# Performance work log

Measured on AMD Instinct MI355X. Metric: run time of the kernel, lower is better.

Reference implementation:

```python
import jax, jax.numpy as jnp
import numpy as np
from jax import lax

LAM = 1.0
B, L = 64, 512
WORD_DIM, POS_DIM, HIDDEN = 256, 32, 768
D_E = 3 * WORD_DIM            # 768, Xe feature dim
D_P = 2 * POS_DIM + WORD_DIM  # 320, Xp feature dim

# fixed piecewise-pool mask table: row 0 = padding, rows 1..3 = segments
MASK_TABLE = jnp.array([[0, 0, 0], [1, 0, 0], [0, 1, 0], [0, 0, 1]], dtype=jnp.float32)


def setup_inputs() -> dict:
    key = jax.random.key(0)
    ks = jax.random.split(key, 9)
    s1 = 1.0 / np.sqrt(D_E)
    s2 = 1.0 / np.sqrt(D_P)
    sc = 1.0 / np.sqrt(D_E * 3)
    return {
        "Xp": jax.random.normal(ks[0], (B, L, D_P), jnp.float32),
        "Xe": jax.random.normal(ks[1], (B, L, D_E), jnp.float32),
        "X_mask": jax.random.randint(ks[2], (B, L), 0, 4, jnp.int32),
        "W1": jax.random.uniform(ks[3], (D_E, D_E), jnp.float32, -s1, s1),
        "b1": jax.random.uniform(ks[4], (D_E,), jnp.float32, -s1, s1),
        "W2": jax.random.uniform(ks[5], (D_E, D_P), jnp.float32, -s2, s2),
        "b2": jax.random.uniform(ks[6], (D_E,), jnp.float32, -s2, s2),
        "Wc": jax.random.uniform(ks[7], (HIDDEN, D_E, 3), jnp.float32, -sc, sc),
        "bc": jax.random.uniform(ks[8], (HIDDEN,), jnp.float32, -sc, sc),
    }


def _forward(Xp, Xe, W1, b1, W2, b2, Wc, bc, X_mask):
    # gated linear fusion of entity and position features
    A = jax.nn.sigmoid(jnp.einsum('bld,od->blo', Xe / LAM, W1) + b1)   # [B,L,D_E]
    X = A * Xe + (1.0 - A) * jnp.tanh(jnp.einsum('bld,od->blo', Xp, W2) + b2)
    # conv1d over length, padding=1 (same)
    x_ncl = jnp.transpose(X, (0, 2, 1))                                 # [B,D_E,L]
    y = lax.conv_general_dilated(x_ncl, Wc, window_strides=(1,),
                                 padding=((1, 1),),
                                 dimension_numbers=('NCH', 'OIH', 'NCH'))
    y = jnp.transpose(y + bc[None, :, None], (0, 2, 1))                 # [B,L,H]
    # piecewise max pooling: mask-multiply then max over L, per segment
    m = MASK_TABLE[X_mask]                                              # [B,L,3]
    pooled = jnp.stack([jnp.max(y * m[:, :, k:k + 1], axis=1) for k in range(3)],
                       axis=-1)                                         # [B,H,3]
    return jnp.tanh(pooled.reshape(-1, HIDDEN * 3))                     # [B,3H]


def reference(Xp, Xe, X_mask, W1, b1, W2, b2, Wc, bc):
    return _forward(Xp, Xe, W1, b1, W2, b2, Wc, bc, X_mask)
```

## Files before the change

kernel.cpp:

```cpp
#include <hip/hip_runtime.h>
#include <math.h>

#define DE 768
#define DP 320
#define HID 768
#define LL 512
#define BB 64
#define M_TOT (BB * LL)
#define HD (HID * DE)

typedef _Float16 half8 __attribute__((ext_vector_type(8)));
typedef _Float16 half4 __attribute__((ext_vector_type(4)));
typedef _Float16 half2v __attribute__((ext_vector_type(2)));
typedef float floatx4 __attribute__((ext_vector_type(4)));

__device__ __forceinline__ void gload16(const void* g, void* l) {
    __builtin_amdgcn_global_load_lds(
        (const __attribute__((address_space(1))) unsigned int*)g,
        (__attribute__((address_space(3))) unsigned int*)l, 16, 0, 0);
}

__device__ __forceinline__ float fast_sigmoid(float x) {
    return __builtin_amdgcn_rcpf(1.f + __expf(-x));
}
__device__ __forceinline__ float fast_tanh(float x) {
    return 2.f * __builtin_amdgcn_rcpf(1.f + __expf(-2.f * x)) - 1.f;
}

__device__ __forceinline__ unsigned fkey(float v) {
    unsigned u = __float_as_uint(v);
    return (u & 0x80000000u) ? ~u : (u | 0x80000000u);
}
__device__ __forceinline__ float funkey(unsigned k) {
    unsigned u = (k & 0x80000000u) ? (k & 0x7FFFFFFFu) : ~k;
    return __uint_as_float(u);
}

__global__ __launch_bounds__(256) void prep_all(
    const float* __restrict__ Xe, const float* __restrict__ W1,
    const float* __restrict__ W2, const float* __restrict__ Wc,
    _Float16* __restrict__ Xe_h, _Float16* __restrict__ W1_h,
    _Float16* __restrict__ W2_h, _Float16* __restrict__ WcT)
{
    const int bid = blockIdx.x, tid = threadIdx.x;
    if (bid < 24576) {
        int idx = bid * 256 + tid;
        float4 v = ((const float4*)Xe)[idx];
        half4 h = {(_Float16)v.x, (_Float16)v.y, (_Float16)v.z, (_Float16)v.w};
        *(half4*)&Xe_h[(size_t)idx * 4] = h;
    } else if (bid < 25152) {
        int idx = (bid - 24576) * 256 + tid;
        float4 v = ((const float4*)W1)[idx];
        half4 h = {(_Float16)v.x, (_Float16)v.y, (_Float16)v.z, (_Float16)v.w};
        *(half4*)&W1_h[(size_t)idx * 4] = h;
    } else if (bid < 25392) {
        int idx = (bid - 25152) * 256 + tid;
        float4 v = ((const float4*)W2)[idx];
        half4 h = {(_Float16)v.x, (_Float16)v.y, (_Float16)v.z, (_Float16)v.w};
        *(half4*)&W2_h[(size_t)idx * 4] = h;
    } else {
        int idx = (bid - 25392) * 256 + tid;
        float a = Wc[(size_t)idx * 3 + 0];
        float b = Wc[(size_t)idx * 3 + 1];
        float c = Wc[(size_t)idx * 3 + 2];
        WcT[idx]          = (_Float16)a;
        WcT[HD + idx]     = (_Float16)b;
        WcT[2 * HD + idx] = (_Float16)c;
    }
}

__global__ __launch_bounds__(256) void gate_kernel(
    const _Float16* __restrict__ Xe_h, const float* __restrict__ Xp,
    const _Float16* __restrict__ W1_h, const float* __restrict__ b1,
    const _Float16* __restrict__ W2_h, const float* __restrict__ b2,
    _Float16* __restrict__ Xout)
{
    __shared__ __align__(16) char smem[24576];
    _Float16 (*As)[32] = (_Float16 (*)[32])smem;
    float    (*Af)[32] = (float (*)[32])smem;
    _Float16 (*Bs)[32] = (_Float16 (*)[32])(smem + 16384);
    unsigned (*Ep)[132] = (unsigned (*)[132])smem;

    const int tid = threadIdx.x;
    const int lane = tid & 63, wid = tid >> 6;
    const int quad = lane >> 4, l15 = lane & 15;
    const int wm = (wid & 1) * 64, wn = (wid >> 1) * 64;
    const int m0 = blockIdx.y * 128, n0 = blockIdx.x * 128;
    const int i4 = lane >> 2, c8 = (lane & 3) * 8;
    const int c8x = c8 ^ ((i4 & 3) * 8);
    const int i8 = lane >> 3, c4 = (lane & 7) * 4;
    const int c4x = c4 ^ ((i8 & 3) * 8);
    const int rsw = (l15 & 3) * 8;

    floatx4 acc[4][4] = {};

    for (int k0 = 0; k0 < DP; k0 += 32) {
        __syncthreads();
        #pragma unroll
        for (int t = 0; t < 4; ++t) {
            int rb = wid * 32 + t * 8;
            gload16(&Xp[(size_t)(m0 + rb + i8) * DP + k0 + c4x], &Af[rb][0]);
        }
        #pragma unroll
        for (int t = 0; t < 2; ++t) {
            int rb = wid * 32 + t * 16;
            gload16(&W2_h[(size_t)(n0 + rb + i4) * DP + k0 + c8x], &Bs[rb][0]);
        }
        __syncthreads();
        half8 af[4], bf[4];
        #pragma unroll
        for (int i = 0; i < 4; ++i) {
            int row = wm + i * 16 + l15;
            int sb = (quad * 8) ^ rsw;
            float4 x0 = *(float4*)&Af[row][sb];
            float4 x1 = *(float4*)&Af[row][sb + 4];
            half8 h = {(_Float16)x0.x, (_Float16)x0.y, (_Float16)x0.z, (_Float16)x0.w,
                       (_Float16)x1.x, (_Float16)x1.y, (_Float16)x1.z, (_Float16)x1.w};
            af[i] = h;
        }
        #pragma unroll
        for (int j = 0; j < 4; ++j)
            bf[j] = *(half8*)&Bs[wn + j * 16 + l15][(quad * 8) ^ rsw];
        #pragma unroll
        for (int i = 0; i < 4; ++i)
            #pragma unroll
            for (int j = 0; j < 4; ++j)
                acc[i][j] = __builtin_amdgcn_mfma_f32_16x16x32_f16(af[i], bf[j], acc[i][j], 0, 0, 0);
    }

    half4 tpk[4][4];
    #pragma unroll
    for (int j = 0; j < 4; ++j) {
        float b2v = b2[n0 + wn + j * 16 + l15];
        #pragma unroll
        for (int i = 0; i < 4; ++i) {
            half4 h;
            #pragma unroll
            for (int r = 0; r < 4; ++r)
                h[r] = (_Float16)fast_tanh(acc[i][j][r] + b2v);
            tpk[i][j] = h;
            acc[i][j] = (floatx4){0.f, 0.f, 0.f, 0.f};
        }
    }

    for (int k0 = 0; k0 < DE; k0 += 32) {
        __syncthreads();
        #pragma unroll
        for (int t = 0; t < 2; ++t) {
            int rb = wid * 32 + t * 16;
            gload16(&Xe_h[(size_t)(m0 + rb + i4) * DE + k0 + c8x], &As[rb][0]);
            gload16(&W1_h[(size_t)(n0 + rb + i4) * DE + k0 + c8x], &Bs[rb][0]);
        }
        __syncthreads();
        half8 af[4], bf[4];
        #pragma unroll
        for (int i = 0; i < 4; ++i)
            af[i] = *(half8*)&As[wm + i * 16 + l15][(quad * 8) ^ rsw];
        #pragma unroll
        for (int j = 0; j < 4; ++j)
            bf[j] = *(half8*)&Bs[wn + j * 16 + l15][(quad * 8) ^ rsw];
        #pragma unroll
        for (int i = 0; i < 4; ++i)
            #pragma unroll
            for (int j = 0; j < 4; ++j)
                acc[i][j] = __builtin_amdgcn_mfma_f32_16x16x32_f16(af[i], bf[j], acc[i][j], 0, 0, 0);
    }

    float b1v[4];
    #pragma unroll
    for (int j = 0; j < 4; ++j) b1v[j] = b1[n0 + wn + j * 16 + l15];

    #pragma unroll
    for (int p = 0; p < 4; ++p) {
        __syncthreads();
        if ((wm >> 6) == (p >> 1)) {
            #pragma unroll
            for (int ii = 0; ii < 2; ++ii) {
                int i = (p & 1) * 2 + ii;
                #pragma unroll
                for (int j = 0; j < 4; ++j) {
                    int col = wn + j * 16 + l15;
                    #pragma unroll
                    for (int r = 0; r < 4; ++r) {
                        int row_l = ii * 16 + quad * 4 + r;
                        float g = fast_sigmoid(acc[i][j][r] + b1v[j]);
                        half2v gt;
                        gt[0] = (_Float16)g;
                        gt[1] = tpk[i][j][r];
                        Ep[row_l][col] = __builtin_bit_cast(unsigned, gt);
                    }
                }
            }
        }
        __syncthreads();
        #pragma unroll
        for (int q = 0; q < 4; ++q) {
            int row_l = q * 8 + (tid >> 5);
            int col = (tid & 31) * 4;
            uint4 w = *(const uint4*)&Ep[row_l][col];
            size_t goff = (size_t)(m0 + p * 32 + row_l) * DE + n0 + col;
            half4 xe4 = *(const half4*)&Xe_h[goff];
            half4 r4;
            #pragma unroll
            for (int e = 0; e < 4; ++e) {
                half2v gt = __builtin_bit_cast(half2v, (&w.x)[e]);
                float g = (float)gt[0], t = (float)gt[1];
                float xe = (float)xe4[e];
                r4[e] = (_Float16)(g * xe + (1.f - g) * t);
            }
            *(half4*)&Xout[goff] = r4;
        }
    }
}

__global__ __launch_bounds__(256) void conv_pool_kernel(
    const _Float16* __restrict__ X, const _Float16* __restrict__ WcT,
    const float* __restrict__ bc, const int* __restrict__ mask,
    unsigned* __restrict__ pool)
{
    __shared__ __align__(16) _Float16 As[144][32];
    __shared__ __align__(16) _Float16 Bs[3][128][32];
    __shared__ unsigned lpool[384];
    __shared__ int smask[128];
    __shared__ int anyNot[3];

    const int tid = threadIdx.x;
    const int lane = tid & 63, wid = tid >> 6;
    const int quad = lane >> 4, l15 = lane & 15;
    const int wm = (wid & 1) * 64, wn = (wid >> 1) * 64;
    const int m0 = blockIdx.y * 128, n0 = blockIdx.x * 128;
    const int b = m0 >> 9, l0 = m0 & 511;
    const int i4 = lane >> 2, c8 = (lane & 3) * 8;
    const int c8x = c8 ^ ((i4 & 3) * 8);
    const int rsw = (l15 & 3) * 8;

    if (tid < 3) anyNot[tid] = 0;
    for (int i = tid; i < 384; i += 256) lpool[i] = 0u;
    if (tid < 128) smask[tid] = mask[b * LL + l0 + tid];
    if (l0 == 0   && tid < 4) *(uint4*)&As[7][tid * 8]   = make_uint4(0u, 0u, 0u, 0u);
    if (l0 == 384 && tid < 4) *(uint4*)&As[136][tid * 8] = make_uint4(0u, 0u, 0u, 0u);
    __syncthreads();
    if (tid < 128) {
        int mv = smask[tid];
        if (mv != 1) atomicOr(&anyNot[0], 1);
        if (mv != 2) atomicOr(&anyNot[1], 1);
        if (mv != 3) atomicOr(&anyNot[2], 1);
    }

    floatx4 acc[4][4] = {};
    for (int k0 = 0; k0 < DE; k0 += 32) {
        __syncthreads();
        #pragma unroll
        for (int t = 0; t < 2; ++t) {
            int c = wid + t * 4;
            int g = l0 - 8 + c * 16 + i4;
            if ((unsigned)g < (unsigned)LL)
                gload16(&X[((size_t)b * LL + g) * DE + k0 + c8x], &As[c * 16][0]);
        }
        if (wid == 0) {
            int g = l0 + 120 + i4;
            if ((unsigned)g < (unsigned)LL)
                gload16(&X[((size_t)b * LL + g) * DE + k0 + c8x], &As[128][0]);
        }
        #pragma unroll
        for (int s = 0; s < 3; ++s) {
            #pragma unroll
            for (int t = 0; t < 2; ++t) {
                int rb = wid * 32 + t * 16;
                gload16(&WcT[(size_t)s * HD + (size_t)(n0 + rb + i4) * DE + k0 + c8x],
                        &Bs[s][rb][0]);
            }
        }
        __syncthreads();
        #pragma unroll
        for (int s = 0; s < 3; ++s) {
            half8 af[4], bf[4];
            #pragma unroll
            for (int i = 0; i < 4; ++i) {
                int pr = wm + i * 16 + l15 + s + 7;
                af[i] = *(half8*)&As[pr][(quad * 8) ^ ((pr & 3) * 8)];
            }
            #pragma unroll
            for (int j = 0; j < 4; ++j)
                bf[j] = *(half8*)&Bs[s][wn + j * 16 + l15][(quad * 8) ^ rsw];
            #pragma unroll
            for (int i = 0; i < 4; ++i)
                #pragma unroll
                for (int j = 0; j < 4; ++j)
                    acc[i][j] = __builtin_amdgcn_mfma_f32_16x16x32_f16(af[i], bf[j], acc[i][j], 0, 0, 0);
        }
    }

    float tmax[4][3];
    #pragma unroll
    for (int j = 0; j < 4; ++j)
        #pragma unroll
        for (int sg = 0; sg < 3; ++sg) tmax[j][sg] = -1e38f;

    #pragma unroll
    for (int i = 0; i < 4; ++i) {
        #pragma unroll
        for (int r = 0; r < 4; ++r) {
            int ll = wm + i * 16 + quad * 4 + r;
            int seg = smask[ll] - 1;
            if (seg >= 0) {
                #pragma unroll
                for (int j = 0; j < 4; ++j)
                    tmax[j][seg] = fmaxf(tmax[j][seg], acc[i][j][r]);
            }
        }
    }
    #pragma unroll
    for (int j = 0; j < 4; ++j) {
        int h = wn + j * 16 + l15;
        float bias = bc[n0 + h];
        #pragma unroll
        for (int sg = 0; sg < 3; ++sg)
            if (tmax[j][sg] > -1e37f)
                atomicMax(&lpool[h * 3 + sg], fkey(tmax[j][sg] + bias));
    }
    __syncthreads();
    for (int i = tid; i < 384; i += 256) {
        int hl = i / 3, k = i - hl * 3;
        unsigned key = lpool[i];
        if (anyNot[k]) {
            unsigned z = fkey(0.0f);
            if (z > key) key = z;
        }
        atomicMax(&pool[((size_t)b * HID + n0 + hl) * 3 + k], key);
    }
}

__global__ void finish_k(const unsigned* __restrict__ pool, float* __restrict__ out) {
    int idx = blockIdx.x * blockDim.x + threadIdx.x;
    if (idx < BB * HID * 3) out[idx] = tanhf(funkey(pool[idx]));
}

extern "C" void kernel_launch(void* const* d_in, const int* in_sizes, int n_in,
                              void* d_out, int out_size, void* d_ws, size_t ws_size,
                              hipStream_t stream) {
    const float* Xp = (const float*)d_in[0];
    const float* Xe = (const float*)d_in[1];
    const int*   Xm = (const int*)d_in[2];
    const float* W1 = (const float*)d_in[3];
    const float* b1 = (const float*)d_in[4];
    const float* W2 = (const float*)d_in[5];
    const float* b2 = (const float*)d_in[6];
    const float* Wc = (const float*)d_in[7];
    const float* bc = (const float*)d_in[8];
    float* out = (float*)d_out;

    _Float16* Xe_h = (_Float16*)d_ws;
    _Float16* X_h  = Xe_h + (size_t)M_TOT * DE;
    _Float16* W1_h = X_h + (size_t)M_TOT * DE;
    _Float16* W2_h = W1_h + (size_t)DE * DE;
    _Float16* WcT  = W2_h + (size_t)DE * DP;
    unsigned* pool = (unsigned*)(WcT + (size_t)3 * HD);

    hipMemsetAsync(pool, 0, (size_t)BB * HID * 3 * sizeof(unsigned), stream);
    prep_all<<<27696, 256, 0, stream>>>(Xe, W1, W2, Wc, Xe_h, W1_h, W2_h, WcT);
    gate_kernel<<<dim3(DE / 128, M_TOT / 128), 256, 0, stream>>>(
        Xe_h, Xp, W1_h, b1, W2_h, b2, X_h);
    conv_pool_kernel<<<dim3(HID / 128, M_TOT / 128), 256, 0, stream>>>(
        X_h, WcT, bc, Xm, pool);
    finish_k<<<(BB * HID * 3 + 255) / 256, 256, 0, stream>>>(pool, out);
}
```

Before: 457.8 us.

## Pre-convert Xp to fp16 and remap GEMM tiles across XCDs

Adds an fp16 conversion of Xp in the prep kernel, when workspace allows, so the gate GEMM loads half-precision A tiles directly instead of fp32 tiles converted in registers. It also remaps block indices in the gate and conv kernels so consecutive blocks on the same XCD share M rows, which is meant to improve L2 reuse. The trade-off is an extra full pass over Xp (read fp32, write fp16) in the prep stage, which may cost more than the gate kernel saves.

```diff
diff --git a/kernel.cpp b/kernel.cpp
--- a/kernel.cpp
+++ b/kernel.cpp
@@ -39,8 +39,10 @@
 __global__ __launch_bounds__(256) void prep_all(
     const float* __restrict__ Xe, const float* __restrict__ W1,
     const float* __restrict__ W2, const float* __restrict__ Wc,
+    const float* __restrict__ Xp,
     _Float16* __restrict__ Xe_h, _Float16* __restrict__ W1_h,
-    _Float16* __restrict__ W2_h, _Float16* __restrict__ WcT)
+    _Float16* __restrict__ W2_h, _Float16* __restrict__ WcT,
+    _Float16* __restrict__ Xp_h)
 {
     const int bid = blockIdx.x, tid = threadIdx.x;
     if (bid < 24576) {
@@ -58,7 +60,7 @@
         float4 v = ((const float4*)W2)[idx];
         half4 h = {(_Float16)v.x, (_Float16)v.y, (_Float16)v.z, (_Float16)v.w};
         *(half4*)&W2_h[(size_t)idx * 4] = h;
-    } else {
+    } else if (bid < 27696) {
         int idx = (bid - 25392) * 256 + tid;
         float a = Wc[(size_t)idx * 3 + 0];
         float b = Wc[(size_t)idx * 3 + 1];
@@ -66,11 +68,18 @@
         WcT[idx]          = (_Float16)a;
         WcT[HD + idx]     = (_Float16)b;
         WcT[2 * HD + idx] = (_Float16)c;
-    }
-}
-
+    } else {
+        int idx = (bid - 27696) * 256 + tid;
+        float4 v = ((const float4*)Xp)[idx];
+        half4 h = {(_Float16)v.x, (_Float16)v.y, (_Float16)v.z, (_Float16)v.w};
+        *(half4*)&Xp_h[(size_t)idx * 4] = h;
+    }
+}
+
+template <bool XPH>
 __global__ __launch_bounds__(256) void gate_kernel(
     const _Float16* __restrict__ Xe_h, const float* __restrict__ Xp,
+    const _Float16* __restrict__ Xp_h,
     const _Float16* __restrict__ W1_h, const float* __restrict__ b1,
     const _Float16* __restrict__ W2_h, const float* __restrict__ b2,
     _Float16* __restrict__ Xout)
@@ -85,7 +94,10 @@
     const int lane = tid & 63, wid = tid >> 6;
     const int quad = lane >> 4, l15 = lane & 15;
     const int wm = (wid & 1) * 64, wn = (wid >> 1) * 64;
-    const int m0 = blockIdx.y * 128, n0 = blockIdx.x * 128;
+    const int linear = blockIdx.y * 6 + blockIdx.x;
+    const int xcd = linear & 7, kk = linear >> 3;
+    const int n0 = (kk % 6) * 128;
+    const int m0 = (xcd * 32 + kk / 6) * 128;
     const int i4 = lane >> 2, c8 = (lane & 3) * 8;
     const int c8x = c8 ^ ((i4 & 3) * 8);
     const int i8 = lane >> 3, c4 = (lane & 7) * 4;
@@ -96,27 +108,42 @@
 
     for (int k0 = 0; k0 < DP; k0 += 32) {
         __syncthreads();
-        #pragma unroll
-        for (int t = 0; t < 4; ++t) {
-            int rb = wid * 32 + t * 8;
-            gload16(&Xp[(size_t)(m0 + rb + i8) * DP + k0 + c4x], &Af[rb][0]);
-        }
-        #pragma unroll
-        for (int t = 0; t < 2; ++t) {
-            int rb = wid * 32 + t * 16;
-            gload16(&W2_h[(size_t)(n0 + rb + i4) * DP + k0 + c8x], &Bs[rb][0]);
+        if (XPH) {
+            #pragma unroll
+            for (int t = 0; t < 2; ++t) {
+                int rb = wid * 32 + t * 16;
+                gload16(&Xp_h[(size_t)(m0 + rb + i4) * DP + k0 + c8x], &As[rb][0]);
+                gload16(&W2_h[(size_t)(n0 + rb + i4) * DP + k0 + c8x], &Bs[rb][0]);
+            }
+        } else {
+            #pragma unroll
+            for (int t = 0; t < 4; ++t) {
+                int rb = wid * 32 + t * 8;
+                gload16(&Xp[(size_t)(m0 + rb + i8) * DP + k0 + c4x], &Af[rb][0]);
+            }
+            #pragma unroll
+            for (int t = 0; t < 2; ++t) {
+                int rb = wid * 32 + t * 16;
+                gload16(&W2_h[(size_t)(n0 + rb + i4) * DP + k0 + c8x], &Bs[rb][0]);
+            }
         }
         __syncthreads();
         half8 af[4], bf[4];
-        #pragma unroll
-        for (int i = 0; i < 4; ++i) {
-            int row = wm + i * 16 + l15;
-            int sb = (quad * 8) ^ rsw;
-            float4 x0 = *(float4*)&Af[row][sb];
-            float4 x1 = *(float4*)&Af[row][sb + 4];
-            half8 h = {(_Float16)x0.x, (_Float16)x0.y, (_Float16)x0.z, (_Float16)x0.w,
-                       (_Float16)x1.x, (_Float16)x1.y, (_Float16)x1.z, (_Float16)x1.w};
-            af[i] = h;
+        if (XPH) {
+            #pragma unroll
+            for (int i = 0; i < 4; ++i)
+                af[i] = *(half8*)&As[wm + i * 16 + l15][(quad * 8) ^ rsw];
+        } else {
+            #pragma unroll
+            for (int i = 0; i < 4; ++i) {
+                int row = wm + i * 16 + l15;
+                int sb = (quad * 8) ^ rsw;
+                float4 x0 = *(float4*)&Af[row][sb];
+                float4 x1 = *(float4*)&Af[row][sb + 4];
+                half8 h = {(_Float16)x0.x, (_Float16)x0.y, (_Float16)x0.z, (_Float16)x0.w,
+                           (_Float16)x1.x, (_Float16)x1.y, (_Float16)x1.z, (_Float16)x1.w};
+                af[i] = h;
+            }
         }
         #pragma unroll
         for (int j = 0; j < 4; ++j)
@@ -228,7 +255,10 @@
     const int lane = tid & 63, wid = tid >> 6;
     const int quad = lane >> 4, l15 = lane & 15;
     const int wm = (wid & 1) * 64, wn = (wid >> 1) * 64;
-    const int m0 = blockIdx.y * 128, n0 = blockIdx.x * 128;
+    const int linear = blockIdx.y * 6 + blockIdx.x;
+    const int xcd = linear & 7, kk = linear >> 3;
+    const int n0 = (kk % 6) * 128;
+    const int m0 = (xcd * 32 + kk / 6) * 128;
     const int b = m0 >> 9, l0 = m0 & 511;
     const int i4 = lane >> 2, c8 = (lane & 3) * 8;
     const int c8x = c8 ^ ((i4 & 3) * 8);
@@ -356,12 +386,22 @@
     _Float16* W2_h = W1_h + (size_t)DE * DE;
     _Float16* WcT  = W2_h + (size_t)DE * DP;
     unsigned* pool = (unsigned*)(WcT + (size_t)3 * HD);
+    _Float16* Xp_h = (_Float16*)(pool + (size_t)BB * HID * 3);
+
+    const size_t need_xph =
+        ((char*)(Xp_h + (size_t)M_TOT * DP)) - (char*)d_ws;
+    const bool use_xph = ws_size >= need_xph;
 
     hipMemsetAsync(pool, 0, (size_t)BB * HID * 3 * sizeof(unsigned), stream);
-    prep_all<<<27696, 256, 0, stream>>>(Xe, W1, W2, Wc, Xe_h, W1_h, W2_h, WcT);
-    gate_kernel<<<dim3(DE / 128, M_TOT / 128), 256, 0, stream>>>(
-        Xe_h, Xp, W1_h, b1, W2_h, b2, X_h);
-    conv_pool_kernel<<<dim3(HID / 128, M_TOT / 128), 256, 0, stream>>>(
+    prep_all<<<use_xph ? 37936 : 27696, 256, 0, stream>>>(
+        Xe, W1, W2, Wc, Xp, Xe_h, W1_h, W2_h, WcT, Xp_h);
+    if (use_xph)
+        gate_kernel<true><<<dim3(6, 256), 256, 0, stream>>>(
+            Xe_h, Xp, Xp_h, W1_h, b1, W2_h, b2, X_h);
+    else
+        gate_kernel<false><<<dim3(6, 256), 256, 0, stream>>>(
+            Xe_h, Xp, Xp_h, W1_h, b1, W2_h, b2, X_h);
+    conv_pool_kernel<<<dim3(6, 256), 256, 0, stream>>>(
         X_h, WcT, bc, Xm, pool);
     finish_k<<<(BB * HID * 3 + 255) / 256, 256, 0, stream>>>(pool, out);
 }
```

After: 434.5 us. -5.1%, faster.
